# Performance work log

Hardware: AMD Instinct MI355X
Metric: run time of the kernel (lower is better)

## Reference

```python
import jax, jax.numpy as jnp
import numpy as np

N = 100000   # nodes
E = 300000   # directed edges (avg degree 3)
F = 3        # num_features
H = 256      # hidden
C = 2        # num_classes
G = 64       # graphs in batch


def setup_inputs() -> dict:
    key = jax.random.key(0)
    ks = jax.random.split(key, 16)
    x = jax.random.normal(ks[0], (N, F), jnp.float32)
    edge_index = jax.random.randint(ks[1], (2, E), 0, N, dtype=jnp.int64)
    batch = jnp.sort(jax.random.randint(ks[2], (N,), 0, G, dtype=jnp.int64))

    def lin(k, fi, fo):
        kw, kb = jax.random.split(k)
        W = jax.random.normal(kw, (fi, fo), jnp.float32) / np.float32(np.sqrt(fi))
        b = jax.random.normal(kb, (fo,), jnp.float32) * 0.01
        return W, b

    W1, b1 = lin(ks[3], F, H)
    W2, b2 = lin(ks[4], H, H)
    W3, b3 = lin(ks[5], H, H)
    W4, b4 = lin(ks[6], H, H)
    W5, b5 = lin(ks[7], H, H)
    Wout, bout = lin(ks[8], H, C)
    return dict(x=x, edge_index=edge_index, batch=batch,
                W1=W1, b1=b1, W2=W2, b2=b2, W3=W3, b3=b3,
                W4=W4, b4=b4, W5=W5, b5=b5, Wout=Wout, bout=bout)


def reference(x, edge_index, batch, W1, b1, W2, b2, W3, b3, W4, b4, W5, b5, Wout, bout):
    n = x.shape[0]
    loops = jnp.arange(n, dtype=edge_index.dtype)
    src = jnp.concatenate([edge_index[0], loops])  # add self-loops (PyG GCNConv)
    dst = jnp.concatenate([edge_index[1], loops])
    # symmetric normalization: deg computed on destination (col) including self-loops
    deg = jax.ops.segment_sum(jnp.ones_like(dst, jnp.float32), dst, num_segments=n)
    dinv = jnp.where(deg > 0, jax.lax.rsqrt(deg), 0.0)
    norm = (dinv[src] * dinv[dst])[:, None]  # [E+N, 1]

    def gcn_conv(h, W, b):
        h = h @ W                                   # linear first (no bias)
        msg = h[src] * norm                         # gather + normalize
        agg = jax.ops.segment_sum(msg, dst, num_segments=n)  # scatter-add
        return agg + b                              # bias after aggregation

    h = jax.nn.relu(gcn_conv(x, W1, b1))            # Dropout(p=0.5) is identity in eval
    for (W, b) in ((W2, b2), (W3, b3), (W4, b4), (W5, b5)):
        h = jax.nn.relu(gcn_conv(h, W, b))

    # global_mean_pool over batch index
    counts = jax.ops.segment_sum(jnp.ones((n,), jnp.float32), batch, num_segments=G)
    pooled = jax.ops.segment_sum(h, batch, num_segments=G) / jnp.maximum(counts, 1.0)[:, None]
    return jax.nn.sigmoid(pooled @ Wout + bout)     # [G, C]
```

## Files before the change

### kernel.cpp

```cpp
#include <hip/hip_runtime.h>
#include <math.h>
#include <stdint.h>

#define H 256
#define EP_STRIDE 264

typedef __attribute__((ext_vector_type(4))) float f32x4;
typedef __attribute__((ext_vector_type(8))) short bf16x8;
typedef __attribute__((ext_vector_type(8))) unsigned short u16x8;

__device__ __forceinline__ float b2f(unsigned short h) { return __uint_as_float(((uint32_t)h) << 16); }
__device__ __forceinline__ unsigned short f2bf(float f) {
    uint32_t u = __float_as_uint(f);
    u = (u + 0x7FFF + ((u >> 16) & 1)) >> 16;
    return (unsigned short)u;
}

__device__ __forceinline__ void gload_lds16(const void* g, void* l) {
    __builtin_amdgcn_global_load_lds(
        (__attribute__((address_space(1))) void*)(uintptr_t)g,
        (__attribute__((address_space(3))) void*)(uint32_t)(uintptr_t)l,
        16, 0, 0);
}

__global__ void k_count(const int* __restrict__ ei, int* __restrict__ deg, int E) {
    int e = blockIdx.x * blockDim.x + threadIdx.x;
    if (e < E) atomicAdd(&deg[ei[E + e]], 1);
}

#define SCAN_B 512
__global__ void k_scan1(const int* __restrict__ deg, int* __restrict__ row_part,
                        int* __restrict__ bsum, float* __restrict__ dinv, int n) {
    __shared__ int sm[SCAN_B];
    int t = threadIdx.x;
    int i = blockIdx.x * SCAN_B + t;
    int v = (i < n) ? deg[i] : 0;
    if (i < n) dinv[i] = rsqrtf((float)(v + 1));
    sm[t] = v;
    __syncthreads();
    for (int off = 1; off < SCAN_B; off <<= 1) {
        int add = (t >= off) ? sm[t - off] : 0;
        __syncthreads();
        sm[t] += add;
        __syncthreads();
    }
    if (i < n) row_part[i] = sm[t] - v;
    if (t == SCAN_B - 1) bsum[blockIdx.x] = sm[t];
}

__global__ void k_scan2(const int* __restrict__ bsum, int* __restrict__ boff, int nb) {
    __shared__ int sm[1024];
    int t = threadIdx.x;
    int v = (t < nb) ? bsum[t] : 0;
    sm[t] = v;
    __syncthreads();
    for (int off = 1; off < 1024; off <<= 1) {
        int add = (t >= off) ? sm[t - off] : 0;
        __syncthreads();
        sm[t] += add;
        __syncthreads();
    }
    if (t < nb) boff[t] = sm[t] - v;
    if (t == 1023) boff[nb] = sm[t];
}

__global__ void k_scan3(int* __restrict__ row_off, const int* __restrict__ row_part,
                        const int* __restrict__ boff, int n, int nb) {
    int i = blockIdx.x * blockDim.x + threadIdx.x;
    if (i < n) row_off[i] = row_part[i] + boff[i >> 9];
    else if (i == n) row_off[n] = boff[nb];
}

__global__ void k_fill(const int* __restrict__ ei, int* __restrict__ cursor,
                       const int* __restrict__ row_off, int* __restrict__ csr, int E) {
    int e = blockIdx.x * blockDim.x + threadIdx.x;
    if (e >= E) return;
    int src = ei[e];
    int dst = ei[E + e];
    int pos = atomicAdd(&cursor[dst], 1);
    csr[row_off[dst] + pos] = src;
}

__global__ void k_wprep(const float* __restrict__ Wa, const float* __restrict__ Wb,
                        const float* __restrict__ Wc, const float* __restrict__ Wd,
                        unsigned short* __restrict__ Wf) {
    int idx = blockIdx.x * 256 + threadIdx.x;
    int l = idx >> 16, rem = idx & 65535;
    int j    = rem & 7;
    int lane = (rem >> 3) & 63;
    int t    = (rem >> 9) & 7;
    int ss   = rem >> 12;
    int g = lane >> 4, r15 = lane & 15;
    int k = t * 32 + g * 8 + j;
    int c = ss * 16 + r15;
    const float* W = (l == 0) ? Wa : (l == 1) ? Wb : (l == 2) ? Wc : Wd;
    Wf[(size_t)l * H * H + rem] = f2bf(W[k * H + c]);
}

__global__ void k_aggx(const float* __restrict__ x, const int* __restrict__ row_off,
                       const int* __restrict__ csr, const float* __restrict__ dinv,
                       float4* __restrict__ u4, int n, int padn) {
    int i = blockIdx.x * blockDim.x + threadIdx.x;
    if (i >= padn) return;
    if (i >= n) { u4[i] = make_float4(0.f, 0.f, 0.f, 0.f); return; }
    float di = dinv[i];
    float a0 = di * x[i * 3 + 0], a1 = di * x[i * 3 + 1], a2 = di * x[i * 3 + 2];
    int ks = row_off[i], ke = row_off[i + 1];
    for (int k = ks; k < ke; k++) {
        int s = csr[k];
        float ds = dinv[s];
        a0 += ds * x[s * 3 + 0];
        a1 += ds * x[s * 3 + 1];
        a2 += ds * x[s * 3 + 2];
    }
    u4[i] = make_float4(a0 * di, a1 * di, a2 * di, 0.f);
}

__device__ __forceinline__ void gemm_body(char* smem, const unsigned short* __restrict__ Wf,
                                          const float* __restrict__ dinv,
                                          unsigned short* __restrict__ out,
                                          int row0, int n, int tid) {
    const int lane = tid & 63;
    const int w = tid >> 6;
    const int g = lane >> 4, r15 = lane & 15;

    bf16x8 af[4][8];
#pragma unroll
    for (int m = 0; m < 4; m++)
#pragma unroll
        for (int t = 0; t < 8; t++)
            af[m][t] = *(const bf16x8*)(smem + ((t * 4 + g) * 64 + m * 16 + r15) * 16);

    float dv[16];
#pragma unroll
    for (int m = 0; m < 4; m++)
#pragma unroll
        for (int j = 0; j < 4; j++) {
            int grow = row0 + m * 16 + g * 4 + j;
            dv[m * 4 + j] = (grow < n) ? dinv[grow] : 0.f;
        }
    __syncthreads();

    const bf16x8* wfrag = (const bf16x8*)Wf;
    unsigned short* ep = (unsigned short*)smem;
#pragma unroll 2
    for (int s = 0; s < 4; s++) {
        int ss = w * 4 + s;
        int col = ss * 16 + r15;
        f32x4 acc[4] = {};
#pragma unroll
        for (int t = 0; t < 8; t++) {
            bf16x8 wf = wfrag[(ss * 8 + t) * 64 + lane];
#pragma unroll
            for (int m = 0; m < 4; m++)
                acc[m] = __builtin_amdgcn_mfma_f32_16x16x32_bf16(af[m][t], wf, acc[m], 0, 0, 0);
        }
#pragma unroll
        for (int m = 0; m < 4; m++)
#pragma unroll
            for (int j = 0; j < 4; j++) {
                int row = m * 16 + g * 4 + j;
                ep[row * EP_STRIDE + col] = f2bf(acc[m][j] * dv[m * 4 + j]);
            }
    }
    __syncthreads();

#pragma unroll
    for (int i = 0; i < 8; i++) {
        int idx = i * 256 + tid;
        int row = idx >> 5, ch = idx & 31;
        u16x8 v = *(const u16x8*)(ep + row * EP_STRIDE + ch * 8);
        *(u16x8*)(out + (size_t)(row0 + row) * H + ch * 8) = v;
    }
}

__global__ __launch_bounds__(256, 2)
void k_gemm(const unsigned short* __restrict__ A, const unsigned short* __restrict__ Wf,
            const float* __restrict__ dinv, unsigned short* __restrict__ out, int n) {
    __shared__ char smem[64 * EP_STRIDE * 2];
    const int tid = threadIdx.x;
    const int lane = tid & 63;
    const int w = tid >> 6;
    const int row0 = (int)blockIdx.x * 64;

    const unsigned short* src = A + (size_t)(row0 + lane) * H;
#pragma unroll
    for (int q = 0; q < 8; q++) {
        int c = w * 8 + q;
        gload_lds16(src + c * 8, smem + (c * 64 + lane) * 16);
    }
    __syncthreads();
    gemm_body(smem, Wf, dinv, out, row0, n, tid);
}

__global__ __launch_bounds__(256, 2)
void k_gemm1(const float4* __restrict__ u4, const float* __restrict__ W1,
             const float* __restrict__ b1, const unsigned short* __restrict__ Wf,
             const float* __restrict__ dinv, unsigned short* __restrict__ out, int n) {
    __shared__ char smem[64 * EP_STRIDE * 2];
    const int tid = threadIdx.x;
    const int row0 = (int)blockIdx.x * 64;
    const int row = tid & 63;
    const int cb = tid >> 6;

    float4 u = u4[row0 + row];
#pragma unroll
    for (int c2 = 0; c2 < 8; c2++) {
        int c = cb * 8 + c2;
        int col0 = c * 8;
        bf16x8 hv;
#pragma unroll
        for (int j = 0; j < 8; j++) {
            int col = col0 + j;
            float v = fmaf(u.x, W1[col], fmaf(u.y, W1[256 + col], fmaf(u.z, W1[512 + col], b1[col])));
            hv[j] = (short)f2bf(fmaxf(v, 0.f));
        }
        *(bf16x8*)(smem + (c * 64 + row) * 16) = hv;
    }
    __syncthreads();
    gemm_body(smem, Wf, dinv, out, row0, n, tid);
}

__global__ void k_agg(const unsigned short* __restrict__ hws, const int* __restrict__ row_off,
                      const int* __restrict__ csr, const float* __restrict__ dinv,
                      const float* __restrict__ bias, unsigned short* __restrict__ out, int n) {
    int node = blockIdx.x * 8 + (threadIdx.x >> 5);
    int cl = threadIdx.x & 31;
    if (node >= n) return;

    float acc[8];
    u16x8 sv = *(const u16x8*)(hws + (size_t)node * H + cl * 8);
#pragma unroll
    for (int j = 0; j < 8; j++) acc[j] = b2f(sv[j]);

    int ks = row_off[node], ke = row_off[node + 1];
    for (int k = ks; k < ke; k += 8) {
        int idx[8];
#pragma unroll
        for (int j = 0; j < 8; j++) idx[j] = (k + j < ke) ? csr[k + j] : -1;
        u16x8 v[8];
#pragma unroll
        for (int j = 0; j < 8; j++)
            if (idx[j] >= 0)
                v[j] = *(const u16x8*)(hws + (size_t)idx[j] * H + cl * 8);
#pragma unroll
        for (int j = 0; j < 8; j++)
            if (idx[j] >= 0) {
#pragma unroll
                for (int q = 0; q < 8; q++) acc[q] += b2f(v[j][q]);
            }
    }

    float4 b0 = ((const float4*)bias)[cl * 2];
    float4 b1v = ((const float4*)bias)[cl * 2 + 1];
    float bb[8] = {b0.x, b0.y, b0.z, b0.w, b1v.x, b1v.y, b1v.z, b1v.w};

    float d = dinv[node];
    u16x8 o;
#pragma unroll
    for (int j = 0; j < 8; j++) o[j] = f2bf(fmaxf(fmaf(acc[j], d, bb[j]), 0.f));
    *(u16x8*)(out + (size_t)node * H + cl * 8) = o;
}

__global__ void k_pool(const unsigned short* __restrict__ h, const int* __restrict__ batch,
                       float* __restrict__ pooled, float* __restrict__ counts, int n) {
    int nb = gridDim.x;
    int per = (n + nb - 1) / nb;
    int s = blockIdx.x * per;
    int e = min(n, s + per);
    if (s >= e) return;
    int t = threadIdx.x;
    float acc = 0.f;
    float cnt = 0.f;
    int cur = batch[s];
    for (int i = s; i < e; i++) {
        int g = batch[i];
        if (g != cur) {
            atomicAdd(&pooled[cur * H + t], acc);
            if (t == 0) atomicAdd(&counts[cur], cnt);
            acc = 0.f; cnt = 0.f; cur = g;
        }
        acc += b2f(h[(size_t)i * H + t]);
        cnt += 1.f;
    }
    atomicAdd(&pooled[cur * H + t], acc);
    if (t == 0) atomicAdd(&counts[cur], cnt);
}

__global__ void k_out(const float* __restrict__ pooled, const float* __restrict__ counts,
                      const float* __restrict__ Wout, const float* __restrict__ bout,
                      float* __restrict__ out, int G) {
    int t = threadIdx.x;
    if (t >= G * 2) return;
    int g = t >> 1, c = t & 1;
    float s = 0.f;
    for (int k = 0; k < H; k++) s = fmaf(pooled[g * H + k], Wout[k * 2 + c], s);
    float cnt = fmaxf(counts[g], 1.0f);
    float logit = s / cnt + bout[c];
    out[g * 2 + c] = 1.f / (1.f + expf(-logit));
}

extern "C" void kernel_launch(void* const* d_in, const int* in_sizes, int n_in,
                              void* d_out, int out_size, void* d_ws, size_t ws_size,
                              hipStream_t stream) {
    const float* x    = (const float*)d_in[0];
    const int*   ei   = (const int*)d_in[1];
    const int*   batch= (const int*)d_in[2];
    const float* W1   = (const float*)d_in[3];
    const float* b1   = (const float*)d_in[4];
    const float* Ws[4] = {(const float*)d_in[5], (const float*)d_in[7],
                          (const float*)d_in[9], (const float*)d_in[11]};
    const float* bs[4] = {(const float*)d_in[6], (const float*)d_in[8],
                          (const float*)d_in[10], (const float*)d_in[12]};
    const float* Wout = (const float*)d_in[13];
    const float* bout = (const float*)d_in[14];

    const int N = in_sizes[0] / 3;
    const int E = in_sizes[1] / 2;
    const int G = out_size / 2;
    const int padN = ((N + 127) / 128) * 128;

    char* p = (char*)d_ws;
    auto alloc = [&](size_t bytes) { char* r = p; p += (bytes + 255) & ~(size_t)255; return r; };
    int*    deg      = (int*)alloc((size_t)N * 4);
    int*    cursor   = (int*)alloc((size_t)N * 4);
    float*  counts   = (float*)alloc((size_t)G * 4);
    float*  pooled   = (float*)alloc((size_t)G * H * 4);
    size_t zero_bytes = (size_t)((char*)p - (char*)d_ws);
    float*  dinv     = (float*)alloc((size_t)N * 4);
    int*    row_part = (int*)alloc((size_t)N * 4);
    int*    row_off  = (int*)alloc((size_t)(N + 1) * 4);
    int*    bsum     = (int*)alloc(1024 * 4);
    int*    boff     = (int*)alloc(1025 * 4);
    int*    csr      = (int*)alloc((size_t)E * 4);
    float4* u4       = (float4*)alloc((size_t)padN * 16);
    unsigned short* Wf   = (unsigned short*)alloc((size_t)4 * H * H * 2);
    unsigned short* bufA = (unsigned short*)alloc((size_t)padN * H * 2);
    unsigned short* bufB = (unsigned short*)alloc((size_t)padN * H * 2);

    hipMemsetAsync(d_ws, 0, zero_bytes, stream);
    k_count<<<(E + 255) / 256, 256, 0, stream>>>(ei, deg, E);

    int nb = (N + SCAN_B - 1) / SCAN_B;
    k_scan1<<<nb, SCAN_B, 0, stream>>>(deg, row_part, bsum, dinv, N);
    k_scan2<<<1, 1024, 0, stream>>>(bsum, boff, nb);
    k_scan3<<<(N + 1 + 255) / 256, 256, 0, stream>>>(row_off, row_part, boff, N, nb);
    k_fill<<<(E + 255) / 256, 256, 0, stream>>>(ei, cursor, row_off, csr, E);

    k_wprep<<<4 * H * H / 256, 256, 0, stream>>>(Ws[0], Ws[1], Ws[2], Ws[3], Wf);

    k_aggx<<<(padN + 255) / 256, 256, 0, stream>>>(x, row_off, csr, dinv, u4, N, padN);

    const int gemmblk = padN / 64;
    const int aggblk  = (N + 7) / 8;

    k_gemm1<<<gemmblk, 256, 0, stream>>>(u4, W1, b1, Wf, dinv, bufA, N);

    for (int l = 0; l < 3; l++) {
        k_agg<<<aggblk, 256, 0, stream>>>(bufA, row_off, csr, dinv, bs[l], bufB, N);
        k_gemm<<<gemmblk, 256, 0, stream>>>(bufB, Wf + (size_t)(l + 1) * H * H, dinv, bufA, N);
    }

    k_agg<<<aggblk, 256, 0, stream>>>(bufA, row_off, csr, dinv, bs[3], bufB, N);
    k_pool<<<1024, 256, 0, stream>>>(bufB, batch, pooled, counts, N);
    k_out<<<1, 256, 0, stream>>>(pooled, counts, Wout, bout, (float*)d_out, G);
}
```

Measured before the change: 400.0 us.

## Make k_gemm persistent with double LDS buffers and prefetch next tile

k_gemm becomes a persistent kernel capped at 512 blocks that loop over 64-row tiles. Each block issues an async global-to-LDS load of its next A tile while it runs the MFMA compute on the current one. The epilogue staging buffer is separated from the A buffer and uses an XOR swizzle in place of padding to avoid LDS bank conflicts. This doubles LDS use per block, which may lower occupancy, and the fixed grid size may not match the CU count.

New measurement: 415.2 us. 3.8% more time.

```diff
diff --git a/kernel.cpp b/kernel.cpp
--- a/kernel.cpp
+++ b/kernel.cpp
@@ -3,7 +3,6 @@
 #include <stdint.h>
 
 #define H 256
-#define EP_STRIDE 264
 
 typedef __attribute__((ext_vector_type(4))) float f32x4;
 typedef __attribute__((ext_vector_type(8))) short bf16x8;
@@ -116,10 +115,12 @@
     u4[i] = make_float4(a0 * di, a1 * di, a2 * di, 0.f);
 }
 
-__device__ __forceinline__ void gemm_body(char* smem, const unsigned short* __restrict__ Wf,
-                                          const float* __restrict__ dinv,
-                                          unsigned short* __restrict__ out,
-                                          int row0, int n, int tid) {
+__device__ __forceinline__ void gemm_compute(char* bufA, char* bufEP,
+                                             const unsigned short* __restrict__ Wf,
+                                             const float* __restrict__ dinv,
+                                             unsigned short* __restrict__ out,
+                                             int row0, int n, int tid, bool prefetch,
+                                             const unsigned short* __restrict__ Asrc_next) {
     const int lane = tid & 63;
     const int w = tid >> 6;
     const int g = lane >> 4, r15 = lane & 15;
@@ -129,7 +130,7 @@
     for (int m = 0; m < 4; m++)
 #pragma unroll
         for (int t = 0; t < 8; t++)
-            af[m][t] = *(const bf16x8*)(smem + ((t * 4 + g) * 64 + m * 16 + r15) * 16);
+            af[m][t] = *(const bf16x8*)(bufA + ((t * 4 + g) * 64 + m * 16 + r15) * 16);
 
     float dv[16];
 #pragma unroll
@@ -141,12 +142,18 @@
         }
     __syncthreads();
 
+    if (prefetch) {
+#pragma unroll
+        for (int q = 0; q < 8; q++) {
+            int c = w * 8 + q;
+            gload_lds16(Asrc_next + c * 8, bufA + (c * 64 + lane) * 16);
+        }
+    }
+
     const bf16x8* wfrag = (const bf16x8*)Wf;
-    unsigned short* ep = (unsigned short*)smem;
 #pragma unroll 2
     for (int s = 0; s < 4; s++) {
         int ss = w * 4 + s;
-        int col = ss * 16 + r15;
         f32x4 acc[4] = {};
 #pragma unroll
         for (int t = 0; t < 8; t++) {
@@ -155,12 +162,14 @@
             for (int m = 0; m < 4; m++)
                 acc[m] = __builtin_amdgcn_mfma_f32_16x16x32_bf16(af[m][t], wf, acc[m], 0, 0, 0);
         }
+        int slot = ((ss * 2 + (r15 >> 3)) ^ (g << 1));
+        int bo = slot * 16 + (r15 & 7) * 2;
 #pragma unroll
         for (int m = 0; m < 4; m++)
 #pragma unroll
             for (int j = 0; j < 4; j++) {
                 int row = m * 16 + g * 4 + j;
-                ep[row * EP_STRIDE + col] = f2bf(acc[m][j] * dv[m * 4 + j]);
+                *(unsigned short*)(bufEP + row * 512 + bo) = f2bf(acc[m][j] * dv[m * 4 + j]);
             }
     }
     __syncthreads();
@@ -169,35 +178,46 @@
     for (int i = 0; i < 8; i++) {
         int idx = i * 256 + tid;
         int row = idx >> 5, ch = idx & 31;
-        u16x8 v = *(const u16x8*)(ep + row * EP_STRIDE + ch * 8);
+        int cw = ch ^ (((row >> 2) & 3) << 1);
+        u16x8 v = *(const u16x8*)(bufEP + row * 512 + cw * 16);
         *(u16x8*)(out + (size_t)(row0 + row) * H + ch * 8) = v;
     }
 }
 
 __global__ __launch_bounds__(256, 2)
 void k_gemm(const unsigned short* __restrict__ A, const unsigned short* __restrict__ Wf,
-            const float* __restrict__ dinv, unsigned short* __restrict__ out, int n) {
-    __shared__ char smem[64 * EP_STRIDE * 2];
+            const float* __restrict__ dinv, unsigned short* __restrict__ out, int n, int nt) {
+    __shared__ char bufA[64 * 512];
+    __shared__ char bufEP[64 * 512];
     const int tid = threadIdx.x;
     const int lane = tid & 63;
     const int w = tid >> 6;
-    const int row0 = (int)blockIdx.x * 64;
-
-    const unsigned short* src = A + (size_t)(row0 + lane) * H;
-#pragma unroll
-    for (int q = 0; q < 8; q++) {
-        int c = w * 8 + q;
-        gload_lds16(src + c * 8, smem + (c * 64 + lane) * 16);
-    }
-    __syncthreads();
-    gemm_body(smem, Wf, dinv, out, row0, n, tid);
+    const int nb = gridDim.x;
+    int t0 = blockIdx.x;
+    if (t0 >= nt) return;
+
+    {
+        const unsigned short* src = A + (size_t)(t0 * 64 + lane) * H;
+#pragma unroll
+        for (int q = 0; q < 8; q++) {
+            int c = w * 8 + q;
+            gload_lds16(src + c * 8, bufA + (c * 64 + lane) * 16);
+        }
+    }
+    for (int t = t0; t < nt; t += nb) {
+        __syncthreads();
+        int tn = t + nb;
+        const unsigned short* srcn = (tn < nt) ? A + (size_t)(tn * 64 + lane) * H : nullptr;
+        gemm_compute(bufA, bufEP, Wf, dinv, out, t * 64, n, tid, tn < nt, srcn);
+    }
 }
 
 __global__ __launch_bounds__(256, 2)
 void k_gemm1(const float4* __restrict__ u4, const float* __restrict__ W1,
              const float* __restrict__ b1, const unsigned short* __restrict__ Wf,
              const float* __restrict__ dinv, unsigned short* __restrict__ out, int n) {
-    __shared__ char smem[64 * EP_STRIDE * 2];
+    __shared__ char bufA[64 * 512];
+    __shared__ char bufEP[64 * 512];
     const int tid = threadIdx.x;
     const int row0 = (int)blockIdx.x * 64;
     const int row = tid & 63;
@@ -215,10 +235,10 @@
             float v = fmaf(u.x, W1[col], fmaf(u.y, W1[256 + col], fmaf(u.z, W1[512 + col], b1[col])));
             hv[j] = (short)f2bf(fmaxf(v, 0.f));
         }
-        *(bf16x8*)(smem + (c * 64 + row) * 16) = hv;
-    }
-    __syncthreads();
-    gemm_body(smem, Wf, dinv, out, row0, n, tid);
+        *(bf16x8*)(bufA + (c * 64 + row) * 16) = hv;
+    }
+    __syncthreads();
+    gemm_compute(bufA, bufEP, Wf, dinv, out, row0, n, tid, false, nullptr);
 }
 
 __global__ void k_agg(const unsigned short* __restrict__ hws, const int* __restrict__ row_off,
@@ -351,14 +371,15 @@
 
     k_aggx<<<(padN + 255) / 256, 256, 0, stream>>>(x, row_off, csr, dinv, u4, N, padN);
 
-    const int gemmblk = padN / 64;
-    const int aggblk  = (N + 7) / 8;
-
-    k_gemm1<<<gemmblk, 256, 0, stream>>>(u4, W1, b1, Wf, dinv, bufA, N);
+    const int nt = padN / 64;
+    const int gemmblk_p = (nt < 512) ? nt : 512;
+    const int aggblk = (N + 7) / 8;
+
+    k_gemm1<<<nt, 256, 0, stream>>>(u4, W1, b1, Wf, dinv, bufA, N);
 
     for (int l = 0; l < 3; l++) {
         k_agg<<<aggblk, 256, 0, stream>>>(bufA, row_off, csr, dinv, bs[l], bufB, N);
-        k_gemm<<<gemmblk, 256, 0, stream>>>(bufB, Wf + (size_t)(l + 1) * H * H, dinv, bufA, N);
+        k_gemm<<<gemmblk_p, 256, 0, stream>>>(bufB, Wf + (size_t)(l + 1) * H * H, dinv, bufA, N, nt);
     }
 
     k_agg<<<aggblk, 256, 0, stream>>>(bufA, row_off, csr, dinv, bs[3], bufB, N);
```
